# Kernel tuning notes

Measured on AMD Instinct MI355X. Metric: run time of the kernel, lower is better.

The kernel has to match this reference:

```python
import jax, jax.numpy as jnp
import numpy as np

D_MODEL = 2048
NUM_HEADS = 16
HEAD_DIM = 128
ROPE_BASE = 10000.0
NEG_INF = -1e9


def setup_inputs() -> dict:
    key = jax.random.key(0)
    ks = jax.random.split(key, 5)
    B, S = 2, 2048
    hidden_states = jax.random.normal(ks[0], (B, S, D_MODEL), dtype=jnp.float32)
    # additive causal mask: 0 on/below diagonal, large-negative above
    causal = jnp.triu(jnp.full((S, S), NEG_INF, dtype=jnp.float32), k=1)
    attention_mask = jnp.broadcast_to(causal, (B, 1, S, S))
    position_ids = jnp.broadcast_to(jnp.arange(S, dtype=jnp.int32), (B, S))
    scale = 1.0 / np.sqrt(D_MODEL)
    Wq = jax.random.normal(ks[1], (D_MODEL, NUM_HEADS * HEAD_DIM), dtype=jnp.float32) * scale
    Wk = jax.random.normal(ks[2], (D_MODEL, NUM_HEADS * HEAD_DIM), dtype=jnp.float32) * scale
    Wv = jax.random.normal(ks[3], (D_MODEL, NUM_HEADS * HEAD_DIM), dtype=jnp.float32) * scale
    Wo = jax.random.normal(ks[4], (NUM_HEADS * HEAD_DIM, D_MODEL), dtype=jnp.float32) * scale
    return {"hidden_states": hidden_states, "attention_mask": attention_mask,
            "position_ids": position_ids, "Wq": Wq, "Wk": Wk, "Wv": Wv, "Wo": Wo}


def _rope_cos_sin(position_ids):
    # inv_freq: [head_dim/2]
    inv_freq = 1.0 / (ROPE_BASE ** (jnp.arange(0, HEAD_DIM, 2, dtype=jnp.float32) / HEAD_DIM))
    freqs = position_ids.astype(jnp.float32)[..., None] * inv_freq  # [B,S,hd/2]
    emb = jnp.concatenate([freqs, freqs], axis=-1)  # [B,S,hd]
    return jnp.cos(emb), jnp.sin(emb)


def _rotate_half(x):
    x1, x2 = jnp.split(x, 2, axis=-1)
    return jnp.concatenate([-x2, x1], axis=-1)


def reference(hidden_states, attention_mask, position_ids, Wq, Wk, Wv, Wo):
    B, S, _ = hidden_states.shape
    H, Dh = NUM_HEADS, HEAD_DIM
    q = (hidden_states @ Wq).reshape(B, S, H, Dh).transpose(0, 2, 1, 3)  # [B,H,S,Dh]
    k = (hidden_states @ Wk).reshape(B, S, H, Dh).transpose(0, 2, 1, 3)
    v = (hidden_states @ Wv).reshape(B, S, H, Dh).transpose(0, 2, 1, 3)
    cos, sin = _rope_cos_sin(position_ids)  # [B,S,Dh]
    cos = cos[:, None, :, :]  # [B,1,S,Dh]
    sin = sin[:, None, :, :]
    q = q * cos + _rotate_half(q) * sin
    k = k * cos + _rotate_half(k) * sin
    scaling = 1.0 / np.sqrt(Dh)
    scores = jnp.einsum('bhqd,bhkd->bhqk', q, k) * scaling  # [B,H,S,S]
    scores = scores + attention_mask[:, :, :, :S]
    attn = jax.nn.softmax(scores.astype(jnp.float32), axis=-1).astype(q.dtype)
    # dropout p=0.0 / eval mode -> identity
    out = jnp.einsum('bhqk,bhkd->bhqd', attn, v)  # [B,H,S,Dh]
    out = out.transpose(0, 2, 1, 3).reshape(B, S, H * Dh)
    return out @ Wo
```

## Files before the change

kernel.cpp:

```cpp
#include <hip/hip_runtime.h>

typedef __attribute__((ext_vector_type(4))) float f32x4;
typedef __attribute__((ext_vector_type(8))) _Float16 f16x8;
typedef __attribute__((ext_vector_type(4))) _Float16 f16x4;

#define SEQ 2048
#define DM 2048
#define NQKV 6144

__device__ __forceinline__ void gload16(const _Float16* g, _Float16* l) {
  __builtin_amdgcn_global_load_lds(
      (const __attribute__((address_space(1))) void*)g,
      (__attribute__((address_space(3))) void*)l, 16, 0, 0);
}

__global__ __launch_bounds__(256) void cvt_x_kernel(const float* __restrict__ X,
                                                    _Float16* __restrict__ Xb, int n4) {
  int i = blockIdx.x * 256 + threadIdx.x;
  if (i < n4) {
    const float4 v = ((const float4*)X)[i];
    f16x4 o;
    o.x = (_Float16)v.x; o.y = (_Float16)v.y; o.z = (_Float16)v.z; o.w = (_Float16)v.w;
    ((f16x4*)Xb)[i] = o;
  }
}

__global__ __launch_bounds__(256) void wtrans_all_kernel(const float* __restrict__ Wq,
                                                         const float* __restrict__ Wk,
                                                         const float* __restrict__ Wv,
                                                         const float* __restrict__ Wo,
                                                         _Float16* __restrict__ Wqkvt,
                                                         _Float16* __restrict__ Wot) {
  __shared__ float tile[64][65];
  const int z = blockIdx.z;
  const float* W = (z == 0) ? Wq : (z == 1) ? Wk : (z == 2) ? Wv : Wo;
  _Float16* Wt = (z < 3) ? (Wqkvt + (size_t)z * 2048 * 2048) : Wot;
  const int n0 = blockIdx.x * 64, k0 = blockIdx.y * 64;
  const int tx = threadIdx.x & 15, ty = threadIdx.x >> 4;
#pragma unroll
  for (int i = 0; i < 4; ++i) {
    const int r = ty + i * 16;
    const float4 v = *(const float4*)&W[(size_t)(k0 + r) * 2048 + n0 + tx * 4];
    tile[r][tx * 4] = v.x; tile[r][tx * 4 + 1] = v.y;
    tile[r][tx * 4 + 2] = v.z; tile[r][tx * 4 + 3] = v.w;
  }
  __syncthreads();
  const int r = threadIdx.x >> 2, u = threadIdx.x & 3;
  _Float16 o[16];
#pragma unroll
  for (int i = 0; i < 16; ++i) o[i] = (_Float16)tile[u * 16 + i][r];
  _Float16* dst = &Wt[(size_t)(n0 + r) * 2048 + k0 + u * 16];
  *(f16x8*)&dst[0] = *(f16x8*)&o[0];
  *(f16x8*)&dst[8] = *(f16x8*)&o[8];
}

__global__ __launch_bounds__(256) void rope_table_kernel(float* __restrict__ ct,
                                                         float* __restrict__ st) {
  int i = blockIdx.x * 256 + threadIdx.x;
  int pos = i >> 6, f = i & 63;
  float inv = powf(10000.0f, -(float)f / 64.0f);
  float ang = (float)pos * inv;
  ct[i] = cosf(ang);
  st[i] = sinf(ang);
}

#define BARX()                                                          \
  do { __builtin_amdgcn_sched_barrier(0); __builtin_amdgcn_s_barrier(); \
       __builtin_amdgcn_sched_barrier(0); } while (0)
#define LGKM0X()                                                        \
  do { asm volatile("s_waitcnt lgkmcnt(0)" ::: "memory");               \
       __builtin_amdgcn_sched_barrier(0); } while (0)

__global__ __launch_bounds__(512, 2) void gemm8q_kernel(
    const _Float16* __restrict__ A, const _Float16* __restrict__ Bt,
    int M, int N, int K, const int* __restrict__ pos_ids,
    const float* __restrict__ ct, const float* __restrict__ st,
    _Float16* __restrict__ Qo, _Float16* __restrict__ Ko,
    _Float16* __restrict__ Vo) {
  __shared__ __align__(16) char smem[135168];
  _Float16* As = (_Float16*)smem;
  _Float16* Bs = (_Float16*)(smem + 65536);
  const int nwg = gridDim.x * gridDim.y;
  const int orig = blockIdx.y * gridDim.x + blockIdx.x;
  const int id = (orig & 7) * (nwg >> 3) + (orig >> 3);
  const int bx = id % gridDim.x, by = id / gridDim.x;
  const int bm = by * 256, bn = bx * 256;
  const int t = threadIdx.x, lane = t & 63, w = t >> 6;
  const int wm = w >> 2, wn = w & 3;
  const int rl = lane & 15, lr4 = lane >> 4;
  const int NKT = K >> 6;

  const int srow = t >> 3;
  const int scol = ((t & 7) ^ (srow & 7)) << 3;
  const _Float16* pA = A + (size_t)(bm + srow) * K + scol;
  const _Float16* pB = Bt + (size_t)(bn + srow) * K + scol;
  _Float16* lA = As + t * 8;
  _Float16* lB = Bs + t * 8;
  const size_t rowK64 = (size_t)64 * K;

#define STA(H, KT, BUF)                                                    \
  { const size_t _g = (size_t)((H) * 128) * K + (size_t)(KT) * 64;         \
    gload16(pA + _g, lA + (BUF) * 16384 + (H) * 8192);                     \
    gload16(pA + _g + rowK64, lA + (BUF) * 16384 + (H) * 8192 + 4096); }
#define STB(H, KT, BUF)                                                    \
  { const size_t _g = (size_t)((H) * 128) * K + (size_t)(KT) * 64;         \
    gload16(pB + _g, lB + (BUF) * 16384 + (H) * 8192);                     \
    gload16(pB + _g + rowK64, lB + (BUF) * 16384 + (H) * 8192 + 4096); }

  const int sw0 = (lr4 ^ (rl & 7)) << 3;
  const int sw1 = ((4 + lr4) ^ (rl & 7)) << 3;
  const int aoff = (wm * 64 + rl) * 64;
  const int boff = (wn * 32 + rl) * 64;

  f16x8 a_[4][2], b0_[2][2], b1_[2][2];
  f32x4 acc[2][2][4][2];
#pragma unroll
  for (int qm = 0; qm < 2; ++qm)
#pragma unroll
    for (int qn = 0; qn < 2; ++qn)
#pragma unroll
      for (int mf = 0; mf < 4; ++mf)
#pragma unroll
        for (int nf = 0; nf < 2; ++nf) acc[qm][qn][mf][nf] = (f32x4)0.0f;

#define LOAD_A(QM, BUF)                                                 \
  { const _Float16* _p = As + (BUF) * 16384 + (QM) * 8192 + aoff;       \
    _Pragma("unroll") for (int mf = 0; mf < 4; ++mf) {                  \
      a_[mf][0] = *(const f16x8*)&_p[mf * 1024 + sw0];                  \
      a_[mf][1] = *(const f16x8*)&_p[mf * 1024 + sw1]; } }
#define LOAD_B(DST, QN, BUF)                                            \
  { const _Float16* _p = Bs + (BUF) * 16384 + (QN) * 8192 + boff;       \
    _Pragma("unroll") for (int nf = 0; nf < 2; ++nf) {                  \
      DST[nf][0] = *(const f16x8*)&_p[nf * 1024 + sw0];                 \
      DST[nf][1] = *(const f16x8*)&_p[nf * 1024 + sw1]; } }
#define MFMA_Q(QM, QN, BREG)                                            \
  __builtin_amdgcn_s_setprio(1);                                        \
  _Pragma("unroll") for (int mf = 0; mf < 4; ++mf)                      \
    _Pragma("unroll") for (int nf = 0; nf < 2; ++nf) {                  \
      acc[QM][QN][mf][nf] = __builtin_amdgcn_mfma_f32_16x16x32_f16(     \
          a_[mf][0], BREG[nf][0], acc[QM][QN][mf][nf], 0, 0, 0);        \
      acc[QM][QN][mf][nf] = __builtin_amdgcn_mfma_f32_16x16x32_f16(     \
          a_[mf][1], BREG[nf][1], acc[QM][QN][mf][nf], 0, 0, 0); }      \
  __builtin_amdgcn_s_setprio(0);

  STA(0, 0, 0); STB(0, 0, 0); STA(1, 0, 0); STB(1, 0, 0);
  STA(0, 1, 1); STB(0, 1, 1); STA(1, 1, 1);
  asm volatile("s_waitcnt vmcnt(6)" ::: "memory");
  BARX();
  LOAD_B(b0_, 0, 0);

  for (int i = 0; i < (NKT >> 1) - 1; ++i) {
    const int k1 = 2 * i + 1, k2 = 2 * i + 2, k3 = 2 * i + 3;
    LOAD_A(0, 0); STB(1, k1, 1);
    BARX(); LGKM0X(); MFMA_Q(0, 0, b0_); BARX();
    LOAD_B(b1_, 1, 0); STA(0, k2, 0);
    BARX(); LGKM0X(); MFMA_Q(0, 1, b1_); BARX();
    LOAD_A(1, 0); STB(0, k2, 0);
    BARX(); LGKM0X(); MFMA_Q(1, 0, b0_); BARX();
    STA(1, k2, 0);
    asm volatile("s_waitcnt vmcnt(6)" ::: "memory");
    BARX();
    MFMA_Q(1, 1, b1_);
    LOAD_B(b0_, 0, 1);
    BARX();
    LOAD_A(0, 1); STB(1, k2, 0);
    BARX(); LGKM0X(); MFMA_Q(0, 0, b0_); BARX();
    LOAD_B(b1_, 1, 1); STA(0, k3, 1);
    BARX(); LGKM0X(); MFMA_Q(0, 1, b1_); BARX();
    LOAD_A(1, 1); STB(0, k3, 1);
    BARX(); LGKM0X(); MFMA_Q(1, 0, b0_); BARX();
    STA(1, k3, 1);
    asm volatile("s_waitcnt vmcnt(6)" ::: "memory");
    BARX();
    MFMA_Q(1, 1, b1_);
    LOAD_B(b0_, 0, 0);
    BARX();
  }
  {
    const int k1 = NKT - 1;
    LOAD_A(0, 0); STB(1, k1, 1);
    BARX(); LGKM0X(); MFMA_Q(0, 0, b0_); BARX();
    LOAD_B(b1_, 1, 0);
    BARX(); LGKM0X(); MFMA_Q(0, 1, b1_); BARX();
    LOAD_A(1, 0);
    BARX(); LGKM0X(); MFMA_Q(1, 0, b0_); BARX();
    asm volatile("s_waitcnt vmcnt(0)" ::: "memory");
    BARX();
    MFMA_Q(1, 1, b1_);
    LOAD_B(b0_, 0, 1);
    BARX();
    LOAD_A(0, 1);
    BARX(); LGKM0X(); MFMA_Q(0, 0, b0_); BARX();
    LOAD_B(b1_, 1, 1);
    BARX(); LGKM0X(); MFMA_Q(0, 1, b1_); BARX();
    LOAD_A(1, 1);
    BARX(); LGKM0X(); MFMA_Q(1, 0, b0_); BARX();
    MFMA_Q(1, 1, b1_);
  }

  const int ttype = bx >> 3;
  const int hh2 = (bx & 7) * 2;
  if (ttype == 2) {
#pragma unroll
    for (int qm = 0; qm < 2; ++qm)
#pragma unroll
      for (int qn = 0; qn < 2; ++qn)
#pragma unroll
        for (int mf = 0; mf < 4; ++mf)
#pragma unroll
          for (int nf = 0; nf < 2; ++nf) {
            const int head = hh2 + qn;
            const int d = wn * 32 + nf * 16 + rl;
            const int s0 = bm + qm * 128 + wm * 64 + mf * 16 + lr4 * 4;
            const int bb = s0 >> 11, ss = s0 & 2047;
            f16x4 v4;
#pragma unroll
            for (int ri = 0; ri < 4; ++ri) v4[ri] = (_Float16)acc[qm][qn][mf][nf][ri];
            *(f16x4*)&Vo[((size_t)(bb * 16 + head) * 128 + d) * SEQ + ss] = v4;
          }
  } else {
    float* cl = (float*)smem;
    LGKM0X();
    BARX();
#pragma unroll
    for (int qm = 0; qm < 2; ++qm) {
#pragma unroll
      for (int qn = 0; qn < 2; ++qn)
#pragma unroll
        for (int mf = 0; mf < 4; ++mf)
#pragma unroll
          for (int nf = 0; nf < 2; ++nf) {
            const int col = qn * 128 + wn * 32 + nf * 16 + rl;
            const int r0 = wm * 64 + mf * 16 + lr4 * 4;
#pragma unroll
            for (int ri = 0; ri < 4; ++ri)
              cl[(r0 + ri) * 264 + col] = acc[qm][qn][mf][nf][ri];
          }
      BARX();
      const int row_l = t >> 2, head_i = (t >> 1) & 1, pb = (t & 1) * 32;
      const int rg = bm + qm * 128 + row_l;
      const int bb = rg >> 11, ss = rg & 2047;
      const int pos = pos_ids[rg];
      const float* cp = ct + pos * 64 + pb;
      const float* sp = st + pos * 64 + pb;
      const int head = hh2 + head_i;
      _Float16* dst = (ttype ? Ko : Qo) + ((size_t)(bb * 16 + head) * SEQ + ss) * 128;
      const float qs = ttype ? 1.0f : 0.08838834764831845f;
      const float* crow = cl + row_l * 264 + head_i * 128;
      _Float16 o1[32], o2[32];
#pragma unroll
      for (int i = 0; i < 32; ++i) {
        const float x1 = crow[pb + i], x2 = crow[pb + 64 + i];
        const float c = cp[i], s = sp[i];
        o1[i] = (_Float16)((x1 * c - x2 * s) * qs);
        o2[i] = (_Float16)((x2 * c + x1 * s) * qs);
      }
#pragma unroll
      for (int i = 0; i < 4; ++i) {
        *(f16x8*)&dst[pb + i * 8] = *(f16x8*)&o1[i * 8];
        *(f16x8*)&dst[pb + 64 + i * 8] = *(f16x8*)&o2[i * 8];
      }
      BARX();
    }
  }
#undef STA
#undef STB
#undef LOAD_A
#undef LOAD_B
#undef MFMA_Q
}

__global__ __launch_bounds__(512, 2) void gemm8n_kernel(
    const _Float16* __restrict__ A, const _Float16* __restrict__ Bt,
    float* __restrict__ Cout, int M, int N, int K) {
  __shared__ __align__(16) _Float16 As[3 * 16384];
  __shared__ __align__(16) _Float16 Bs[3 * 8192];
  const int nwg = gridDim.x * gridDim.y;
  const int orig = blockIdx.y * gridDim.x + blockIdx.x;
  const int id = (orig & 7) * (nwg >> 3) + (orig >> 3);
  const int bx = id % gridDim.x, by = id / gridDim.x;
  const int bm = by * 256, bn = bx * 128;
  const int t = threadIdx.x, lane = t & 63, w = t >> 6;
  const int wm = w >> 2, wn = w & 3;
  const int rl = lane & 15, lr4 = lane >> 4;
  const int NKT = K >> 6;

  const int srow = t >> 3;
  const int scol = ((t & 7) ^ (srow & 7)) << 3;
  const _Float16* pA = A + (size_t)(bm + srow) * K + scol;
  const _Float16* pB = Bt + (size_t)(bn + srow) * K + scol;
  _Float16* lA = As + t * 8;
  _Float16* lB = Bs + t * 8;
  const size_t rowK64 = (size_t)64 * K;

#define STA(H, KT, SLOT)                                                   \
  { const size_t _g = (size_t)((H) * 128) * K + (size_t)(KT) * 64;         \
    gload16(pA + _g, lA + (SLOT) * 16384 + (H) * 8192);                    \
    gload16(pA + _g + rowK64, lA + (SLOT) * 16384 + (H) * 8192 + 4096); }
#define STB(KT, SLOT)                                                      \
  { const size_t _g = (size_t)(KT) * 64;                                   \
    gload16(pB + _g, lB + (SLOT) * 8192);                                  \
    gload16(pB + _g + rowK64, lB + (SLOT) * 8192 + 4096); }

  const int sw0 = (lr4 ^ (rl & 7)) << 3;
  const int sw1 = ((4 + lr4) ^ (rl & 7)) << 3;
  const int aoff = (wm * 64 + rl) * 64;
  const int boff = (wn * 32 + rl) * 64;

  f16x8 a_[4][2], b_[2][2];
  f32x4 acc[2][4][2];
#pragma unroll
  for (int qm = 0; qm < 2; ++qm)
#pragma unroll
    for (int mf = 0; mf < 4; ++mf)
#pragma unroll
      for (int nf = 0; nf < 2; ++nf) acc[qm][mf][nf] = (f32x4)0.0f;

#define LOAD_A(H, SLOT)                                                 \
  { const _Float16* _p = As + (SLOT) * 16384 + (H) * 8192 + aoff;       \
    _Pragma("unroll") for (int mf = 0; mf < 4; ++mf) {                  \
      a_[mf][0] = *(const f16x8*)&_p[mf * 1024 + sw0];                  \
      a_[mf][1] = *(const f16x8*)&_p[mf * 1024 + sw1]; } }
#define LOAD_B(SLOT)                                                    \
  { const _Float16* _p = Bs + (SLOT) * 8192 + boff;                     \
    _Pragma("unroll") for (int nf = 0; nf < 2; ++nf) {                  \
      b_[nf][0] = *(const f16x8*)&_p[nf * 1024 + sw0];                  \
      b_[nf][1] = *(const f16x8*)&_p[nf * 1024 + sw1]; } }
#define MFMA_Q(QM)                                                      \
  __builtin_amdgcn_s_setprio(1);                                        \
  _Pragma("unroll") for (int mf = 0; mf < 4; ++mf)                      \
    _Pragma("unroll") for (int nf = 0; nf < 2; ++nf) {                  \
      acc[QM][mf][nf] = __builtin_amdgcn_mfma_f32_16x16x32_f16(         \
          a_[mf][0], b_[nf][0], acc[QM][mf][nf], 0, 0, 0);              \
      acc[QM][mf][nf] = __builtin_amdgcn_mfma_f32_16x16x32_f16(         \
          a_[mf][1], b_[nf][1], acc[QM][mf][nf], 0, 0, 0); }            \
  __builtin_amdgcn_s_setprio(0);
#define VM6() asm volatile("s_waitcnt vmcnt(6)" ::: "memory")
#define VM0() asm volatile("s_waitcnt vmcnt(0)" ::: "memory")

  STA(0, 0, 0); STB(0, 0); STA(1, 0, 0);
  STA(0, 1, 1); STB(1, 1); STA(1, 1, 1);
  VM6();
  BARX();

  for (int jb = 0; jb + 4 < NKT; jb += 3) {
    LOAD_A(0, 0); LOAD_B(0); STA(0, jb + 2, 2); STB(jb + 2, 2);
    BARX(); LGKM0X(); MFMA_Q(0); BARX();
    LOAD_A(1, 0); STA(1, jb + 2, 2);
    VM6(); BARX(); LGKM0X(); MFMA_Q(1); BARX();
    LOAD_A(0, 1); LOAD_B(1); STA(0, jb + 3, 0); STB(jb + 3, 0);
    BARX(); LGKM0X(); MFMA_Q(0); BARX();
    LOAD_A(1, 1); STA(1, jb + 3, 0);
    VM6(); BARX(); LGKM0X(); MFMA_Q(1); BARX();
    LOAD_A(0, 2); LOAD_B(2); STA(0, jb + 4, 1); STB(jb + 4, 1);
    BARX(); LGKM0X(); MFMA_Q(0); BARX();
    LOAD_A(1, 2); STA(1, jb + 4, 1);
    VM6(); BARX(); LGKM0X(); MFMA_Q(1); BARX();
  }
  {
    LOAD_A(0, 0); LOAD_B(0);
    BARX(); LGKM0X(); MFMA_Q(0); BARX();
    LOAD_A(1, 0);
    VM0();
    BARX(); LGKM0X(); MFMA_Q(1); BARX();
    LOAD_A(0, 1); LOAD_B(1);
    BARX(); LGKM0X(); MFMA_Q(0); BARX();
    LOAD_A(1, 1);
    BARX(); LGKM0X(); MFMA_Q(1);
  }

#pragma unroll
  for (int qm = 0; qm < 2; ++qm)
#pragma unroll
    for (int mf = 0; mf < 4; ++mf)
#pragma unroll
      for (int nf = 0; nf < 2; ++nf) {
        const int col = bn + wn * 32 + nf * 16 + rl;
#pragma unroll
        for (int ri = 0; ri < 4; ++ri) {
          const int row = bm + qm * 128 + wm * 64 + mf * 16 + lr4 * 4 + ri;
          Cout[(size_t)row * N + col] = acc[qm][mf][nf][ri];
        }
      }
#undef STA
#undef STB
#undef LOAD_A
#undef LOAD_B
#undef MFMA_Q
#undef VM6
#undef VM0
}

__global__ __launch_bounds__(512) void attn_kernel(const _Float16* __restrict__ Q,
                                                   const _Float16* __restrict__ K,
                                                   const _Float16* __restrict__ Vt,
                                                   _Float16* __restrict__ O) {
  __shared__ __align__(16) _Float16 Ks[2][128 * 128];
  __shared__ __align__(16) _Float16 Vs[2][128 * 128];
  __shared__ __align__(16) _Float16 Ps[8][16 * 128];
  const int bh = blockIdx.x;
  const int pair = blockIdx.y;
  const int b = bh >> 4, h = bh & 15;
  const int t = threadIdx.x, lane = t & 63, w = t >> 6;
  const int lr = lane >> 4, lc = lane & 15;
  const _Float16* Qb = Q + (size_t)bh * SEQ * 128;
  const _Float16* Kb = K + (size_t)bh * SEQ * 128;
  const _Float16* Vb = Vt + (size_t)bh * 128 * SEQ;

  f16x8 onef;
#pragma unroll
  for (int i = 0; i < 8; ++i) onef[i] = (_Float16)1.0f;

  auto stage = [&](int buf, int kb) {
    const int k0 = kb * 128;
#pragma unroll
    for (int i = 0; i < 4; ++i) {
      const int c = i * 512 + t;
      const int row = c >> 4, u = c & 15;
      gload16(&Kb[(size_t)(k0 + row) * 128 + ((u ^ (row & 7)) << 3)], &Ks[buf][c * 8]);
    }
#pragma unroll
    for (int i = 0; i < 4; ++i) {
      const int c = i * 512 + t;
      const int dim = c >> 4, u = c & 15;
      gload16(&Vb[(size_t)dim * SEQ + k0 + ((u ^ (dim & 7)) << 3)], &Vs[buf][c * 8]);
    }
  };

  for (int half = 0; half < 2; ++half) {
    const int j = half ? (15 - pair) : pair;
    const int q0 = j * 128;
    const int nkb = j + 1;
    const int rowmin = q0 + w * 16;

    f16x8 qf[4];
    {
      const int qrow = q0 + w * 16 + lc;
#pragma unroll
      for (int kk = 0; kk < 4; ++kk)
        qf[kk] = *(const f16x8*)&Qb[(size_t)qrow * 128 + kk * 32 + lr * 8];
    }
    f32x4 acco[8];
#pragma unroll
    for (int i = 0; i < 8; ++i) acco[i] = (f32x4)0.0f;
    float l_r[4] = {0.f, 0.f, 0.f, 0.f};

    stage(0, 0);
    for (int kb = 0; kb < nkb; ++kb) {
      const int cur = kb & 1;
      const bool more = kb + 1 < nkb;
      if (more) {
        stage(cur ^ 1, kb + 1);
        asm volatile("s_waitcnt vmcnt(8)" ::: "memory");
      } else {
        asm volatile("s_waitcnt vmcnt(0)" ::: "memory");
      }
      BARX();
      const int k0 = kb * 128;
      if (k0 <= rowmin + 15) {
        f32x4 sacc[8];
#pragma unroll
        for (int jj = 0; jj < 8; ++jj) sacc[jj] = (f32x4)0.0f;
#pragma unroll
        for (int jj = 0; jj < 8; ++jj) {
          const int krow = jj * 16 + lc;
#pragma unroll
          for (int kk = 0; kk < 4; ++kk) {
            const int idx = (krow * 128 + kk * 32 + lr * 8) ^ ((krow & 7) << 3);
            f16x8 kf = *(const f16x8*)&Ks[cur][idx];
            sacc[jj] = __builtin_amdgcn_mfma_f32_16x16x32_f16(qf[kk], kf, sacc[jj], 0, 0, 0);
          }
        }
        const bool diag = (k0 + 127 > rowmin);
#pragma unroll
        for (int r = 0; r < 4; ++r) {
          const int rowi = rowmin + lr * 4 + r;
          const int rbase = (lr * 4 + r) * 128;
          const int rsw = ((lr * 4 + r) & 7) << 3;
#pragma unroll
          for (int jj = 0; jj < 8; ++jj) {
            float sv = sacc[jj][r];
            if (diag && (k0 + jj * 16 + lc > rowi)) sv = -1e30f;
            const float pv = __expf(sv);
            Ps[w][rbase + ((jj * 16 + lc) ^ rsw)] = (_Float16)pv;
          }
        }
        const int csw = (lc & 7) << 3;
        f16x8 pf[4];
#pragma unroll
        for (int c = 0; c < 4; ++c)
          pf[c] = *(const f16x8*)&Ps[w][lc * 128 + ((c * 32 + lr * 8) ^ csw)];
        f32x4 psum = (f32x4)0.0f;
#pragma unroll
        for (int c = 0; c < 4; ++c)
          psum = __builtin_amdgcn_mfma_f32_16x16x32_f16(pf[c], onef, psum, 0, 0, 0);
#pragma unroll
        for (int tt = 0; tt < 8; ++tt) {
          const int dim = tt * 16 + lc;
          const int dsw = (dim & 7) << 3;
#pragma unroll
          for (int c = 0; c < 4; ++c) {
            const int vidx = (dim * 128 + c * 32 + lr * 8) ^ dsw;
            acco[tt] = __builtin_amdgcn_mfma_f32_16x16x32_f16(
                pf[c], *(const f16x8*)&Vs[cur][vidx], acco[tt], 0, 0, 0);
          }
        }
#pragma unroll
        for (int r = 0; r < 4; ++r) l_r[r] += psum[r];
      }
      BARX();
    }
#pragma unroll
    for (int tt = 0; tt < 8; ++tt) {
      const int col = h * 128 + tt * 16 + lc;
#pragma unroll
      for (int r = 0; r < 4; ++r) {
        const int row = q0 + w * 16 + lr * 4 + r;
        O[(size_t)(b * SEQ + row) * DM + col] = (_Float16)(acco[tt][r] / l_r[r]);
      }
    }
  }
}

extern "C" void kernel_launch(void* const* d_in, const int* in_sizes, int n_in,
                              void* d_out, int out_size, void* d_ws, size_t ws_size,
                              hipStream_t stream) {
  const float* hidden = (const float*)d_in[0];
  const int* pos_ids = (const int*)d_in[2];
  const float* Wq = (const float*)d_in[3];
  const float* Wk = (const float*)d_in[4];
  const float* Wv = (const float*)d_in[5];
  const float* Wo = (const float*)d_in[6];

  char* ws = (char*)d_ws;
  _Float16* Xb    = (_Float16*)(ws + 0);
  _Float16* Wqkvt = (_Float16*)(ws + 16777216);
  _Float16* Wot   = (_Float16*)(ws + 41943040);
  _Float16* Qbuf  = (_Float16*)(ws + 50331648);
  _Float16* Kbuf  = (_Float16*)(ws + 67108864);
  _Float16* Vtbuf = (_Float16*)(ws + 83886080);
  _Float16* Obuf  = (_Float16*)(ws + 100663296);
  float* ct       = (float*)(ws + 117440512);
  float* st       = (float*)(ws + 117964800);

  cvt_x_kernel<<<8192, 256, 0, stream>>>(hidden, Xb, 2097152);
  wtrans_all_kernel<<<dim3(32, 32, 4), 256, 0, stream>>>(Wq, Wk, Wv, Wo, Wqkvt, Wot);
  rope_table_kernel<<<512, 256, 0, stream>>>(ct, st);

  gemm8q_kernel<<<dim3(24, 16), 512, 0, stream>>>(
      Xb, Wqkvt, 4096, 6144, 2048, pos_ids, ct, st, Qbuf, Kbuf, Vtbuf);

  attn_kernel<<<dim3(32, 8), 512, 0, stream>>>(Qbuf, Kbuf, Vtbuf, Obuf);

  gemm8n_kernel<<<dim3(16, 16), 512, 0, stream>>>(
      Obuf, Wot, (float*)d_out, 4096, 2048, 2048);
}
```

Baseline: 256.1 us.

## Switch attention to 32x32x16 MFMA with shared P tile across waves

Reworks the attention kernel so the 8 waves form 4 row groups times 2 key/dim halves and use 32x32x16 MFMA instead of 16x16x32. Each wave computes a 32x64 score slice, writes exp values into one shared 128x128 P tile, then after a barrier reads full P rows to do the PV product for its half of the head dimension. The goal is fewer LDS reads per MFMA and larger MFMA tiles. In exchange it adds a block-wide barrier per key block and drops the per-wave skip of fully masked tiles, and the row sum is now computed redundantly by both dim-half waves.

```diff
diff --git a/kernel.cpp b/kernel.cpp
--- a/kernel.cpp
+++ b/kernel.cpp
@@ -1,6 +1,7 @@
 #include <hip/hip_runtime.h>
 
 typedef __attribute__((ext_vector_type(4))) float f32x4;
+typedef __attribute__((ext_vector_type(16))) float f32x16;
 typedef __attribute__((ext_vector_type(8))) _Float16 f16x8;
 typedef __attribute__((ext_vector_type(4))) _Float16 f16x4;
 
@@ -397,12 +398,13 @@
                                                    _Float16* __restrict__ O) {
   __shared__ __align__(16) _Float16 Ks[2][128 * 128];
   __shared__ __align__(16) _Float16 Vs[2][128 * 128];
-  __shared__ __align__(16) _Float16 Ps[8][16 * 128];
+  __shared__ __align__(16) _Float16 Ps[128 * 128];
   const int bh = blockIdx.x;
   const int pair = blockIdx.y;
   const int b = bh >> 4, h = bh & 15;
   const int t = threadIdx.x, lane = t & 63, w = t >> 6;
-  const int lr = lane >> 4, lc = lane & 15;
+  const int rowgrp = w & 3, kh = w >> 2;
+  const int l31 = lane & 31, l5 = lane >> 5;
   const _Float16* Qb = Q + (size_t)bh * SEQ * 128;
   const _Float16* Kb = K + (size_t)bh * SEQ * 128;
   const _Float16* Vb = Vt + (size_t)bh * 128 * SEQ;
@@ -431,25 +433,19 @@
     const int j = half ? (15 - pair) : pair;
     const int q0 = j * 128;
     const int nkb = j + 1;
-    const int rowmin = q0 + w * 16;
-
-    f16x8 qf[4];
-    {
-      const int qrow = q0 + w * 16 + lc;
-#pragma unroll
-      for (int kk = 0; kk < 4; ++kk)
-        qf[kk] = *(const f16x8*)&Qb[(size_t)qrow * 128 + kk * 32 + lr * 8];
-    }
-    f32x4 acco[8];
-#pragma unroll
-    for (int i = 0; i < 8; ++i) acco[i] = (f32x4)0.0f;
-    float l_r[4] = {0.f, 0.f, 0.f, 0.f};
+
+    const int qrow = q0 + rowgrp * 32 + l31;
+    f16x8 qf[8];
+#pragma unroll
+    for (int kc = 0; kc < 8; ++kc)
+      qf[kc] = *(const f16x8*)&Qb[(size_t)qrow * 128 + kc * 16 + l5 * 8];
+
+    f32x16 acco0 = (f32x16)0.0f, acco1 = (f32x16)0.0f, lsum = (f32x16)0.0f;
 
     stage(0, 0);
     for (int kb = 0; kb < nkb; ++kb) {
       const int cur = kb & 1;
-      const bool more = kb + 1 < nkb;
-      if (more) {
+      if (kb + 1 < nkb) {
         stage(cur ^ 1, kb + 1);
         asm volatile("s_waitcnt vmcnt(8)" ::: "memory");
       } else {
@@ -457,67 +453,58 @@
       }
       BARX();
       const int k0 = kb * 128;
-      if (k0 <= rowmin + 15) {
-        f32x4 sacc[8];
-#pragma unroll
-        for (int jj = 0; jj < 8; ++jj) sacc[jj] = (f32x4)0.0f;
-#pragma unroll
-        for (int jj = 0; jj < 8; ++jj) {
-          const int krow = jj * 16 + lc;
-#pragma unroll
-          for (int kk = 0; kk < 4; ++kk) {
-            const int idx = (krow * 128 + kk * 32 + lr * 8) ^ ((krow & 7) << 3);
-            f16x8 kf = *(const f16x8*)&Ks[cur][idx];
-            sacc[jj] = __builtin_amdgcn_mfma_f32_16x16x32_f16(qf[kk], kf, sacc[jj], 0, 0, 0);
-          }
+      f32x16 sacc0 = (f32x16)0.0f, sacc1 = (f32x16)0.0f;
+      const int key0 = kh * 64 + l31;
+      const int ksw = (l31 & 7) << 3;
+#pragma unroll
+      for (int kc = 0; kc < 8; ++kc) {
+        const int off = kc * 16 + l5 * 8;
+        sacc0 = __builtin_amdgcn_mfma_f32_32x32x16_f16(
+            qf[kc], *(const f16x8*)&Ks[cur][key0 * 128 + (off ^ ksw)], sacc0, 0, 0, 0);
+        sacc1 = __builtin_amdgcn_mfma_f32_32x32x16_f16(
+            qf[kc], *(const f16x8*)&Ks[cur][(key0 + 32) * 128 + (off ^ ksw)], sacc1, 0, 0, 0);
+      }
+#pragma unroll
+      for (int kb2 = 0; kb2 < 2; ++kb2) {
+        const int key_l = kh * 64 + kb2 * 32 + l31;
+#pragma unroll
+        for (int reg = 0; reg < 16; ++reg) {
+          const int row_l = rowgrp * 32 + (reg & 3) + 8 * (reg >> 2) + 4 * l5;
+          float sv = kb2 ? sacc1[reg] : sacc0[reg];
+          if (k0 + key_l > q0 + row_l) sv = -1e30f;
+          Ps[row_l * 128 + (key_l ^ ((row_l & 7) << 3))] = (_Float16)__expf(sv);
         }
-        const bool diag = (k0 + 127 > rowmin);
-#pragma unroll
-        for (int r = 0; r < 4; ++r) {
-          const int rowi = rowmin + lr * 4 + r;
-          const int rbase = (lr * 4 + r) * 128;
-          const int rsw = ((lr * 4 + r) & 7) << 3;
-#pragma unroll
-          for (int jj = 0; jj < 8; ++jj) {
-            float sv = sacc[jj][r];
-            if (diag && (k0 + jj * 16 + lc > rowi)) sv = -1e30f;
-            const float pv = __expf(sv);
-            Ps[w][rbase + ((jj * 16 + lc) ^ rsw)] = (_Float16)pv;
-          }
-        }
-        const int csw = (lc & 7) << 3;
-        f16x8 pf[4];
-#pragma unroll
-        for (int c = 0; c < 4; ++c)
-          pf[c] = *(const f16x8*)&Ps[w][lc * 128 + ((c * 32 + lr * 8) ^ csw)];
-        f32x4 psum = (f32x4)0.0f;
-#pragma unroll
-        for (int c = 0; c < 4; ++c)
-          psum = __builtin_amdgcn_mfma_f32_16x16x32_f16(pf[c], onef, psum, 0, 0, 0);
-#pragma unroll
-        for (int tt = 0; tt < 8; ++tt) {
-          const int dim = tt * 16 + lc;
-          const int dsw = (dim & 7) << 3;
-#pragma unroll
-          for (int c = 0; c < 4; ++c) {
-            const int vidx = (dim * 128 + c * 32 + lr * 8) ^ dsw;
-            acco[tt] = __builtin_amdgcn_mfma_f32_16x16x32_f16(
-                pf[c], *(const f16x8*)&Vs[cur][vidx], acco[tt], 0, 0, 0);
-          }
-        }
-#pragma unroll
-        for (int r = 0; r < 4; ++r) l_r[r] += psum[r];
+      }
+      LGKM0X();
+      BARX();
+      const int prow = rowgrp * 32 + l31;
+      const int psw = (l31 & 7) << 3;
+      f16x8 pA[8];
+#pragma unroll
+      for (int kc = 0; kc < 8; ++kc)
+        pA[kc] = *(const f16x8*)&Ps[prow * 128 + ((kc * 16 + l5 * 8) ^ psw)];
+#pragma unroll
+      for (int kc = 0; kc < 8; ++kc)
+        lsum = __builtin_amdgcn_mfma_f32_32x32x16_f16(pA[kc], onef, lsum, 0, 0, 0);
+      const int d0 = kh * 64 + l31;
+      const int dsw = (l31 & 7) << 3;
+#pragma unroll
+      for (int kc = 0; kc < 8; ++kc) {
+        const int off = kc * 16 + l5 * 8;
+        acco0 = __builtin_amdgcn_mfma_f32_32x32x16_f16(
+            pA[kc], *(const f16x8*)&Vs[cur][d0 * 128 + (off ^ dsw)], acco0, 0, 0, 0);
+        acco1 = __builtin_amdgcn_mfma_f32_32x32x16_f16(
+            pA[kc], *(const f16x8*)&Vs[cur][(d0 + 32) * 128 + (off ^ dsw)], acco1, 0, 0, 0);
       }
       BARX();
     }
 #pragma unroll
-    for (int tt = 0; tt < 8; ++tt) {
-      const int col = h * 128 + tt * 16 + lc;
-#pragma unroll
-      for (int r = 0; r < 4; ++r) {
-        const int row = q0 + w * 16 + lr * 4 + r;
-        O[(size_t)(b * SEQ + row) * DM + col] = (_Float16)(acco[tt][r] / l_r[r]);
-      }
+    for (int reg = 0; reg < 16; ++reg) {
+      const int row = q0 + rowgrp * 32 + (reg & 3) + 8 * (reg >> 2) + 4 * l5;
+      const float inv = 1.0f / lsum[reg];
+      _Float16* orow = &O[(size_t)(b * SEQ + row) * DM + h * 128 + kh * 64 + l31];
+      orow[0] = (_Float16)(acco0[reg] * inv);
+      orow[32] = (_Float16)(acco1[reg] * inv);
     }
   }
 }
```

Measured after the change: 251.5 us. No clear change (-1.8%).
